# Performance work log

Hardware: AMD Instinct MI355X
Metric: run time of the kernel (lower is better)

The kernel has to match this reference:

```python
import jax, jax.numpy as jnp
import numpy as np

V, E, D, H = 50000, 800000, 128, 128  # nodes, edges, node_feat_size, graph_feat_size
NEG_SLOPE = 0.01  # nn.LeakyReLU default


def setup_inputs() -> dict:
    key = jax.random.key(0)
    ks = jax.random.split(key, 11)
    s = 0.05
    return {
        "node_feats": jax.random.normal(ks[0], (V, D), jnp.float32),
        "W_edge": jax.random.normal(ks[1], (1, 2 * D), jnp.float32) * s,
        "b_edge": jnp.zeros((1,), jnp.float32),
        "W_proj": jax.random.normal(ks[2], (H, D), jnp.float32) * s,
        "b_proj": jnp.zeros((H,), jnp.float32),
        "W_ih": jax.random.normal(ks[3], (3 * D, H), jnp.float32) * s,
        "W_hh": jax.random.normal(ks[4], (3 * D, D), jnp.float32) * s,
        "b_ih": jnp.zeros((3 * D,), jnp.float32),
        "b_hh": jnp.zeros((3 * D,), jnp.float32),
        "src": jax.random.randint(ks[5], (E,), 0, V),
        "dst": jax.random.randint(ks[6], (E,), 0, V),
    }


def _leaky_relu(x):
    return jnp.where(x >= 0, x, NEG_SLOPE * x)


def _edge_softmax(logits, dst, num_nodes):
    # segment softmax over edges grouped by destination node; logits: [E, 1]
    m = jax.ops.segment_max(logits, dst, num_segments=num_nodes)
    m = jnp.where(jnp.isfinite(m), m, 0.0)  # guard empty segments
    e = jnp.exp(logits - m[dst])
    s = jax.ops.segment_sum(e, dst, num_segments=num_nodes)
    return e / s[dst]


def reference(node_feats, W_edge, b_edge, W_proj, b_proj, W_ih, W_hh, b_ih, b_hh, src, dst):
    # GNNLayer.apply_edges: he = cat([dst_feat, src_feat])  [E, 2D]
    he = jnp.concatenate([node_feats[dst], node_feats[src]], axis=1)
    # project_edge: Dropout (eval: identity) -> Linear(2D, 1) -> LeakyReLU
    logits = _leaky_relu(he @ W_edge.T + b_edge)  # [E, 1]
    # AttentiveGRU2: edge_softmax per dst
    a = _edge_softmax(logits, dst, V)  # [E, 1]
    # project_node: Dropout (eval) -> Linear(D, H)
    hv = node_feats @ W_proj.T + b_proj  # [V, H]
    # src_mul_edge + sum aggregation to dst
    m = hv[src] * a  # [E, H]
    c = jax.ops.segment_sum(m, dst, num_segments=V)  # [V, H]
    context = jax.nn.elu(c)
    # PyTorch GRUCell(context, node_feats)
    gi = context @ W_ih.T + b_ih      # [V, 3D]
    gh = node_feats @ W_hh.T + b_hh   # [V, 3D]
    i_r, i_z, i_n = jnp.split(gi, 3, axis=1)
    h_r, h_z, h_n = jnp.split(gh, 3, axis=1)
    r = jax.nn.sigmoid(i_r + h_r)
    z = jax.nn.sigmoid(i_z + h_z)
    n = jnp.tanh(i_n + r * h_n)
    h_new = (1.0 - z) * n + z * node_feats
    return jax.nn.relu(h_new)
```

## Files before the change

kernel.cpp:

```cpp
#include <hip/hip_runtime.h>
#include <hip/hip_bf16.h>


#define V_NODES 50000
#define E_EDGES 800000
#define D_FEAT  128
#define GCHUNK  5
#define WS_BLOCKS 1250
#define GRU_BLOCKS 1264

#define NCHUNK  49
#define CHUNK_E 16384
#define RANGES  4
#define NODE_R  12500
#define HISTG   (NCHUNK * RANGES)
#define SCAN_BLOCKS 196

typedef short bf16x8 __attribute__((ext_vector_type(8)));
typedef float f32x4  __attribute__((ext_vector_type(4)));
typedef unsigned short u16x4 __attribute__((ext_vector_type(4)));

#define OFF_WEDGE 0
#define OFF_WPROJ 256
#define OFF_WIH   16640
#define OFF_WHH   65792
#define OFF_BEDGE 114944
#define OFF_BPROJ 114945
#define OFF_BIH   115073
#define OFF_BHH   115457
#define SMALL_TOTAL 115841
#define CONV_X_BLOCKS   6250
#define CONV_S_BLOCKS   453
#define HIST_BLOCKS     3125

__device__ int   g_is_bf16;
__device__ float g_pd[V_NODES];
__device__ float g_ps[V_NODES];
__device__ __attribute__((aligned(16))) unsigned int g_mat[NCHUNK * V_NODES];
__device__ int   g_row_off[V_NODES + 1];
__device__ int   g_blocksum[SCAN_BLOCKS];
__device__ unsigned short g_rank16[E_EDGES];
__device__ __attribute__((aligned(16))) int2 g_s_pair[E_EDGES];
__device__ __attribute__((aligned(16))) unsigned short g_xbf[V_NODES * D_FEAT];
__device__ __attribute__((aligned(16))) unsigned short g_wsmall[SMALL_TOTAL + 15];
__device__ __attribute__((aligned(16))) unsigned short g_hv[V_NODES * D_FEAT];
__device__ __attribute__((aligned(16))) unsigned short g_ctx[V_NODES * D_FEAT];

static __device__ __forceinline__ float b2f(unsigned short u) {
  union { unsigned int i; float f; } v; v.i = ((unsigned int)u) << 16; return v.f;
}
static __device__ __forceinline__ unsigned short f2b(float f) {
  unsigned int i = __float_as_uint(f);
  unsigned int r = (i + 0x7FFFu + ((i >> 16) & 1u)) >> 16;
  return (unsigned short)r;
}
static __device__ __forceinline__ bf16x8 load_frag(const unsigned short* p) {
  return *reinterpret_cast<const bf16x8*>(p);
}
static __device__ __forceinline__ float fast_rcp(float x) {
  return __builtin_amdgcn_rcpf(x);
}
static __device__ __forceinline__ float fast_sigmoid(float x) {
  return fast_rcp(1.f + __expf(-x));
}
static __device__ __forceinline__ float fast_tanh(float y) {
  return 1.f - 2.f * fast_rcp(__expf(2.f * y) + 1.f);
}
static __device__ __forceinline__ void async_copy16(const void* g, void* l) {
  __builtin_amdgcn_global_load_lds(
      (const __attribute__((address_space(1))) void*)g,
      (__attribute__((address_space(3))) void*)l, 16, 0, 0);
}

__global__ void probe_kernel(const unsigned int* __restrict__ x)
{
  __shared__ int cnt;
  if (threadIdx.x == 0) cnt = 0;
  __syncthreads();
  const unsigned int w  = x[threadIdx.x];
  const unsigned int lo = w & 0xFFFFu;
  const unsigned int ex = (lo >> 7) & 0xFFu;
  if (lo != 0u && ex >= 118u && ex <= 132u) atomicAdd(&cnt, 1);
  __syncthreads();
  if (threadIdx.x == 0) g_is_bf16 = (cnt >= 200) ? 1 : 0;
}

__global__ void conv_fused_kernel(
    const void* __restrict__ x,
    const void* p0, const void* p1, const void* p2, const void* p3,
    const void* p4, const void* p5, const void* p6, const void* p7)
{
  const int b = blockIdx.x;
  if (b < CONV_X_BLOCKS) {
    const int t = b * 256 + threadIdx.x;
    if (g_is_bf16) {
      reinterpret_cast<u16x4*>(g_xbf)[t] = reinterpret_cast<const u16x4*>(x)[t];
    } else {
      const float4 v = reinterpret_cast<const float4*>(x)[t];
      u16x4 o; o.x = f2b(v.x); o.y = f2b(v.y); o.z = f2b(v.z); o.w = f2b(v.w);
      reinterpret_cast<u16x4*>(g_xbf)[t] = o;
    }
  } else {
    const int i = (b - CONV_X_BLOCKS) * 256 + threadIdx.x;
    if (i >= SMALL_TOTAL) return;
    const int offs[9] = {OFF_WEDGE, OFF_WPROJ, OFF_WIH, OFF_WHH,
                         OFF_BEDGE, OFF_BPROJ, OFF_BIH, OFF_BHH, SMALL_TOTAL};
    const void* ps[8] = {p0, p1, p2, p3, p4, p5, p6, p7};
    int r = 0;
#pragma unroll
    for (int k = 0; k < 8; k++) if (i >= offs[k]) r = k;
    const int j = i - offs[r];
    g_wsmall[i] = g_is_bf16
        ? reinterpret_cast<const unsigned short*>(ps[r])[j]
        : f2b(reinterpret_cast<const float*>(ps[r])[j]);
  }
}

__global__ __launch_bounds__(256, 2) void np_hist_kernel(const int* __restrict__ dst)
{
  __shared__ unsigned int hloc[NODE_R / 2];
  __shared__ __attribute__((aligned(16))) char lds_x[2][4096];
  const int b = blockIdx.x;
  if (b < HISTG) {
    const int c  = b >> 2;
    const int r0 = (b & 3) * NODE_R;
    for (int i = threadIdx.x; i < NODE_R / 2; i += 256) hloc[i] = 0u;
    __syncthreads();
    const int ebase = c * CHUNK_E;
    const int ecnt  = min(CHUNK_E, E_EDGES - ebase);
    const int4* dst4 = reinterpret_cast<const int4*>(dst + ebase);
    const int n4 = ecnt >> 2;
    for (int i = threadIdx.x; i < n4; i += 256) {
      const int4 d4 = dst4[i];
      const int e0 = ebase + (i << 2);
      const unsigned int rx = (unsigned int)(d4.x - r0);
      const unsigned int ry = (unsigned int)(d4.y - r0);
      const unsigned int rz = (unsigned int)(d4.z - r0);
      const unsigned int rw = (unsigned int)(d4.w - r0);
      if (rx < (unsigned int)NODE_R) {
        const unsigned int sh = (rx & 1u) << 4;
        const unsigned int old = atomicAdd(&hloc[rx >> 1], 1u << sh);
        g_rank16[e0] = (unsigned short)((old >> sh) & 0xFFFFu);
      }
      if (ry < (unsigned int)NODE_R) {
        const unsigned int sh = (ry & 1u) << 4;
        const unsigned int old = atomicAdd(&hloc[ry >> 1], 1u << sh);
        g_rank16[e0 + 1] = (unsigned short)((old >> sh) & 0xFFFFu);
      }
      if (rz < (unsigned int)NODE_R) {
        const unsigned int sh = (rz & 1u) << 4;
        const unsigned int old = atomicAdd(&hloc[rz >> 1], 1u << sh);
        g_rank16[e0 + 2] = (unsigned short)((old >> sh) & 0xFFFFu);
      }
      if (rw < (unsigned int)NODE_R) {
        const unsigned int sh = (rw & 1u) << 4;
        const unsigned int old = atomicAdd(&hloc[rw >> 1], 1u << sh);
        g_rank16[e0 + 3] = (unsigned short)((old >> sh) & 0xFFFFu);
      }
    }
    __syncthreads();
    uint2* mout = reinterpret_cast<uint2*>(&g_mat[c * V_NODES + r0]);
    for (int i = threadIdx.x; i < NODE_R / 2; i += 256) {
      const unsigned int w = hloc[i];
      mout[i] = make_uint2(w & 0xFFFFu, w >> 16);
    }
    return;
  }
  const int wid   = threadIdx.x >> 6;
  const int g     = (b - HISTG) * 4 + wid;
  const int lane  = threadIdx.x & 63;
  const int cg    = g & 7;
  const int chunk = g >> 3;
  const int col   = lane & 15;
  const int quad  = lane >> 4;
  const int h     = 16 * cg + col;

  bf16x8 bw[4];
#pragma unroll
  for (int kk = 0; kk < 4; kk++)
    bw[kk] = load_frag(g_wsmall + OFF_WPROJ + h * D_FEAT + kk * 32 + quad * 8);
  bf16x8 be[4];
#pragma unroll
  for (int kk = 0; kk < 4; kk++) { be[kk] = bf16x8{0,0,0,0,0,0,0,0}; }
  if (cg == 0 && col < 2) {
#pragma unroll
    for (int kk = 0; kk < 4; kk++)
      be[kk] = load_frag(g_wsmall + OFF_WEDGE + col * D_FEAT + kk * 32 + quad * 8);
  }
  const float bp = b2f(g_wsmall[OFF_BPROJ + h]);

  const int o_lin = wid * 1024 + lane * 16;
  const int o_src = o_lin ^ (((o_lin >> 8) & 7) << 4);
  const char* xbf_b = reinterpret_cast<const char*>(g_xbf);

  const int t0 = chunk * GCHUNK;
  async_copy16(xbf_b + (size_t)t0 * 4096 + o_src, &lds_x[0][wid * 1024]);

  for (int i = 0; i < GCHUNK; i++) {
    const int t = t0 + i;
    const int buf = i & 1;
    __syncthreads();
    bf16x8 a[4];
#pragma unroll
    for (int kk = 0; kk < 4; kk++) {
      const int phys = (col * 256 + kk * 64 + quad * 16) ^ ((col & 7) << 4);
      a[kk] = *reinterpret_cast<const bf16x8*>(&lds_x[buf][phys]);
    }
    if (i + 1 < GCHUNK)
      async_copy16(xbf_b + (size_t)(t + 1) * 4096 + o_src,
                   &lds_x[buf ^ 1][wid * 1024]);
    f32x4 acc; acc[0]=0.f; acc[1]=0.f; acc[2]=0.f; acc[3]=0.f;
#pragma unroll
    for (int kk = 0; kk < 4; kk++)
      acc = __builtin_amdgcn_mfma_f32_16x16x32_bf16(a[kk], bw[kk], acc, 0, 0, 0);
#pragma unroll
    for (int r = 0; r < 4; r++)
      g_hv[(t * 16 + quad * 4 + r) * D_FEAT + h] = f2b(acc[r] + bp);
    if (cg == 0) {
      f32x4 acce; acce[0]=0.f; acce[1]=0.f; acce[2]=0.f; acce[3]=0.f;
#pragma unroll
      for (int kk = 0; kk < 4; kk++)
        acce = __builtin_amdgcn_mfma_f32_16x16x32_bf16(a[kk], be[kk], acce, 0, 0, 0);
      if (col == 0) {
#pragma unroll
        for (int r = 0; r < 4; r++) g_pd[t * 16 + quad * 4 + r] = acce[r];
      } else if (col == 1) {
#pragma unroll
        for (int r = 0; r < 4; r++) g_ps[t * 16 + quad * 4 + r] = acce[r];
      }
    }
  }
}

__global__ __launch_bounds__(256) void scan_a_kernel()
{
  __shared__ int lds[256];
  const int b = blockIdx.x, t = threadIdx.x;
  const int idx = b * 256 + t;
  int v = 0;
  if (idx < V_NODES) {
#pragma unroll 7
    for (int c = 0; c < NCHUNK; c++) v += (int)g_mat[c * V_NODES + idx];
  }
  lds[t] = v;
  __syncthreads();
  for (int off = 1; off < 256; off <<= 1) {
    int tmp = (t >= off) ? lds[t - off] : 0;
    __syncthreads();
    lds[t] += tmp;
    __syncthreads();
  }
  if (idx < V_NODES) g_row_off[idx] = lds[t] - v;
  if (t == 255) g_blocksum[b] = lds[255];
}

__global__ __launch_bounds__(256) void scan_bcm_kernel()
{
  __shared__ int lds[256];
  const int b = blockIdx.x, t = threadIdx.x;
  const int v = (t < SCAN_BLOCKS) ? g_blocksum[t] : 0;
  lds[t] = v;
  __syncthreads();
  for (int off = 1; off < 256; off <<= 1) {
    int tmp = (t >= off) ? lds[t - off] : 0;
    __syncthreads();
    lds[t] += tmp;
    __syncthreads();
  }
  const int total = lds[255];
  const int boff  = (b == 0) ? 0 : lds[b - 1];
  const int idx = b * 256 + t;
  if (idx < V_NODES) {
    int running = g_row_off[idx] + boff;
    g_row_off[idx] = running;
#pragma unroll 7
    for (int c = 0; c < NCHUNK; c++) {
      const unsigned int cnt = g_mat[c * V_NODES + idx];
      g_mat[c * V_NODES + idx] = (unsigned int)running;
      running += (int)cnt;
    }
  }
  if (b == 0 && t == 0) g_row_off[V_NODES] = total;
}

__global__ void edge_scatter_kernel(
    const int* __restrict__ src, const int* __restrict__ dst, int E)
{
  int e = blockIdx.x * blockDim.x + threadIdx.x;
  if (e >= E) return;
  const int d = dst[e], sn = src[e];
  float logit = g_pd[d] + g_ps[sn] + b2f(g_wsmall[OFF_BEDGE]);
  logit = (logit >= 0.f) ? logit : 0.01f * logit;
  const float w = __expf(logit);
  const int c = e >> 14;
  const int pos = (int)g_mat[c * V_NODES + d] + (int)g_rank16[e];
  g_s_pair[pos] = make_int2(sn, __float_as_int(w));
}

__global__ __launch_bounds__(256) void aggregate_kernel()
{
  const int v = blockIdx.x * 4 + (threadIdx.x >> 6);
  const int lane = threadIdx.x & 63;
  const int beg = g_row_off[v], end = g_row_off[v + 1];
  float accx = 0.f, accy = 0.f, ssum = 0.f;
  int i = beg;
  for (; i + 8 <= end; i += 8) {
    int2 q[8];
#pragma unroll
    for (int j = 0; j < 8; j++) q[j] = g_s_pair[i + j];
    unsigned int p[8];
#pragma unroll
    for (int j = 0; j < 8; j++)
      p[j] = *reinterpret_cast<const unsigned int*>(g_hv + q[j].x * D_FEAT + lane * 2);
#pragma unroll
    for (int j = 0; j < 8; j++) {
      const float w = __int_as_float(q[j].y);
      ssum += w;
      accx += w * b2f((unsigned short)(p[j] & 0xFFFFu));
      accy += w * b2f((unsigned short)(p[j] >> 16));
    }
  }
  for (; i + 4 <= end; i += 4) {
    int2 q[4];
#pragma unroll
    for (int j = 0; j < 4; j++) q[j] = g_s_pair[i + j];
    unsigned int p[4];
#pragma unroll
    for (int j = 0; j < 4; j++)
      p[j] = *reinterpret_cast<const unsigned int*>(g_hv + q[j].x * D_FEAT + lane * 2);
#pragma unroll
    for (int j = 0; j < 4; j++) {
      const float w = __int_as_float(q[j].y);
      ssum += w;
      accx += w * b2f((unsigned short)(p[j] & 0xFFFFu));
      accy += w * b2f((unsigned short)(p[j] >> 16));
    }
  }
  for (; i < end; i++) {
    const int2 q = g_s_pair[i];
    const float w = __int_as_float(q.y);
    ssum += w;
    const unsigned int pair =
        *reinterpret_cast<const unsigned int*>(g_hv + q.x * D_FEAT + lane * 2);
    accx += w * b2f((unsigned short)(pair & 0xFFFFu));
    accy += w * b2f((unsigned short)(pair >> 16));
  }
  const float inv = (end > beg) ? (1.0f / ssum) : 0.0f;
  float c0 = accx * inv, c1 = accy * inv;
  c0 = (c0 > 0.f) ? c0 : (__expf(c0) - 1.f);
  c1 = (c1 > 0.f) ? c1 : (__expf(c1) - 1.f);
  const unsigned int outp = ((unsigned int)f2b(c1) << 16) | (unsigned int)f2b(c0);
  *reinterpret_cast<unsigned int*>(g_ctx + v * D_FEAT + lane * 2) = outp;
}

__global__ __launch_bounds__(256, 2) void gru_kernel(const float* __restrict__ xf32,
                                                     float* __restrict__ out)
{
  const int d = blockIdx.x;
  const int x = d & 7;
  const int s = d >> 3;
  const int chunk = x + 8 * (s >> 1);
  if (chunk >= 625) return;
  __shared__ __attribute__((aligned(16))) char lds_s[2][8192];
  const int half  = s & 1;
  const int wid   = threadIdx.x >> 6;
  const int lane  = threadIdx.x & 63;
  const int cg    = half * 4 + wid;
  const int col   = lane & 15;
  const int quad  = lane >> 4;
  const int h     = 16 * cg + col;
  const unsigned short* W_ih = g_wsmall + OFF_WIH;
  const unsigned short* W_hh = g_wsmall + OFF_WHH;
  const int isb = g_is_bf16;

  const float br  = b2f(g_wsmall[OFF_BIH + h])       + b2f(g_wsmall[OFF_BHH + h]);
  const float bz  = b2f(g_wsmall[OFF_BIH + 128 + h]) + b2f(g_wsmall[OFF_BHH + 128 + h]);
  const float bn  = b2f(g_wsmall[OFF_BIH + 256 + h]);
  const float bh_ = b2f(g_wsmall[OFF_BHH + 256 + h]);

  bf16x8 bIHr[4], bHHr[4], bIHz[4], bHHz[4], bIHn[4], bHHn[4];
#pragma unroll
  for (int kk = 0; kk < 4; kk++) {
    const int ko = kk * 32 + quad * 8;
    bIHr[kk] = load_frag(W_ih + h * D_FEAT + ko);
    bHHr[kk] = load_frag(W_hh + h * D_FEAT + ko);
    bIHz[kk] = load_frag(W_ih + (128 + h) * D_FEAT + ko);
    bHHz[kk] = load_frag(W_hh + (128 + h) * D_FEAT + ko);
    bIHn[kk] = load_frag(W_ih + (256 + h) * D_FEAT + ko);
    bHHn[kk] = load_frag(W_hh + (256 + h) * D_FEAT + ko);
  }

  const int o_lin = wid * 1024 + lane * 16;
  const int o_src = o_lin ^ (((o_lin >> 8) & 7) << 4);
  const char* xbf_b = reinterpret_cast<const char*>(g_xbf);
  const char* ctx_b = reinterpret_cast<const char*>(g_ctx);

  const int t0 = chunk * GCHUNK;
  async_copy16(xbf_b + (size_t)t0 * 4096 + o_src, &lds_s[0][wid * 1024]);
  async_copy16(ctx_b + (size_t)t0 * 4096 + o_src, &lds_s[0][4096 + wid * 1024]);

  for (int i = 0; i < GCHUNK; i++) {
    const int t = t0 + i;
    const int buf = i & 1;
    __syncthreads();
    bf16x8 ax[4], ac[4];
#pragma unroll
    for (int kk = 0; kk < 4; kk++) {
      const int phys = (col * 256 + kk * 64 + quad * 16) ^ ((col & 7) << 4);
      ax[kk] = *reinterpret_cast<const bf16x8*>(&lds_s[buf][phys]);
      ac[kk] = *reinterpret_cast<const bf16x8*>(&lds_s[buf][4096 + phys]);
    }
    if (i + 1 < GCHUNK) {
      async_copy16(xbf_b + (size_t)(t + 1) * 4096 + o_src,
                   &lds_s[buf ^ 1][wid * 1024]);
      async_copy16(ctx_b + (size_t)(t + 1) * 4096 + o_src,
                   &lds_s[buf ^ 1][4096 + wid * 1024]);
    }
    float xv[4];
    if (isb) {
#pragma unroll
      for (int r = 0; r < 4; r++)
        xv[r] = b2f(g_xbf[(t * 16 + quad * 4 + r) * D_FEAT + h]);
    } else {
#pragma unroll
      for (int r = 0; r < 4; r++)
        xv[r] = xf32[(t * 16 + quad * 4 + r) * D_FEAT + h];
    }
    f32x4 racc, zacc, niacc, nhacc;
    racc[0]=br;  racc[1]=br;  racc[2]=br;  racc[3]=br;
    zacc[0]=bz;  zacc[1]=bz;  zacc[2]=bz;  zacc[3]=bz;
    niacc[0]=bn; niacc[1]=bn; niacc[2]=bn; niacc[3]=bn;
    nhacc[0]=bh_; nhacc[1]=bh_; nhacc[2]=bh_; nhacc[3]=bh_;
#pragma unroll
    for (int kk = 0; kk < 4; kk++) {
      racc  = __builtin_amdgcn_mfma_f32_16x16x32_bf16(ac[kk], bIHr[kk], racc, 0, 0, 0);
      racc  = __builtin_amdgcn_mfma_f32_16x16x32_bf16(ax[kk], bHHr[kk], racc, 0, 0, 0);
      zacc  = __builtin_amdgcn_mfma_f32_16x16x32_bf16(ac[kk], bIHz[kk], zacc, 0, 0, 0);
      zacc  = __builtin_amdgcn_mfma_f32_16x16x32_bf16(ax[kk], bHHz[kk], zacc, 0, 0, 0);
      niacc = __builtin_amdgcn_mfma_f32_16x16x32_bf16(ac[kk], bIHn[kk], niacc, 0, 0, 0);
      nhacc = __builtin_amdgcn_mfma_f32_16x16x32_bf16(ax[kk], bHHn[kk], nhacc, 0, 0, 0);
    }
#pragma unroll
    for (int r = 0; r < 4; r++) {
      const int vrow = t * 16 + quad * 4 + r;
      const float rg = fast_sigmoid(racc[r]);
      const float zg = fast_sigmoid(zacc[r]);
      const float n  = fast_tanh(niacc[r] + rg * nhacc[r]);
      const float hn = (1.f - zg) * n + zg * xv[r];
      out[vrow * D_FEAT + h] = (hn < 0.f) ? 0.f : hn;
    }
  }
}

extern "C" void kernel_launch(void* const* d_in, const int* in_sizes, int n_in,
                              void* d_out, int out_size, void* d_ws, size_t ws_size,
                              hipStream_t stream)
{
  (void)d_ws; (void)ws_size; (void)out_size;

  int ix = -1, iWe = -1, ibe = -1, iWp = -1, ibp = -1,
      iWih = -1, iWhh = -1, ibih = -1, ibhh = -1, isrc = -1, idst = -1;
  for (int i = 0; i < n_in; i++) {
    const int s = in_sizes[i];
    if      (s == 6400000) ix = i;
    else if (s == 256)     iWe = i;
    else if (s == 1)       ibe = i;
    else if (s == 16384)   iWp = i;
    else if (s == 128)     ibp = i;
    else if (s == 49152)   { if (iWih < 0) iWih = i; else iWhh = i; }
    else if (s == 384)     { if (ibih < 0) ibih = i; else ibhh = i; }
    else if (s == 800000)  { if (isrc < 0) isrc = i; else idst = i; }
  }
  if (ix < 0 || iWe < 0 || ibe < 0 || iWp < 0 || ibp < 0 || iWih < 0 ||
      iWhh < 0 || ibih < 0 || ibhh < 0 || isrc < 0 || idst < 0) {
    ix = 0; iWe = 1; ibe = 2; iWp = 3; ibp = 4;
    iWih = 5; iWhh = 6; ibih = 7; ibhh = 8; isrc = 9; idst = 10;
  }

  const int* src = (const int*)d_in[isrc];
  const int* dst = (const int*)d_in[idst];
  float* out = (float*)d_out;

  probe_kernel<<<1, 256, 0, stream>>>((const unsigned int*)d_in[ix]);
  conv_fused_kernel<<<CONV_X_BLOCKS + CONV_S_BLOCKS, 256, 0, stream>>>(
      d_in[ix],
      d_in[iWe], d_in[iWp], d_in[iWih], d_in[iWhh],
      d_in[ibe], d_in[ibp], d_in[ibih], d_in[ibhh]);
  np_hist_kernel<<<HISTG + WS_BLOCKS, 256, 0, stream>>>(dst);
  scan_a_kernel<<<SCAN_BLOCKS, 256, 0, stream>>>();
  scan_bcm_kernel<<<SCAN_BLOCKS, 256, 0, stream>>>();
  edge_scatter_kernel<<<HIST_BLOCKS, 256, 0, stream>>>(src, dst, E_EDGES);
  aggregate_kernel<<<V_NODES / 4, 256, 0, stream>>>();
  gru_kernel<<<GRU_BLOCKS, 256, 0, stream>>>((const float*)d_in[ix], out);
}
```

Baseline: 207.2 us.

## Inline dtype probe per block, fuse conversion with histogram, deepen aggregate unroll

Removes the single-block probe kernel by having every conversion block and every GRU block recompute the bf16/fp32 detection locally from the first 256 input words. The dst histogram moves out of the node-projection kernel into the conversion kernel, so histogramming runs alongside format conversion and one launch plus one global flag disappear. The aggregate loop's gather batch grows from 8 to 12 edges to keep more loads in flight. In exchange every block pays an extra barrier pair and a small read, and the larger unroll raises register pressure.

```diff
diff --git a/kernel.cpp b/kernel.cpp
--- a/kernel.cpp
+++ b/kernel.cpp
@@ -33,7 +33,6 @@
 #define CONV_S_BLOCKS   453
 #define HIST_BLOCKS     3125
 
-__device__ int   g_is_bf16;
 __device__ float g_pd[V_NODES];
 __device__ float g_ps[V_NODES];
 __device__ __attribute__((aligned(16))) unsigned int g_mat[NCHUNK * V_NODES];
@@ -71,103 +70,104 @@
       (const __attribute__((address_space(1))) void*)g,
       (__attribute__((address_space(3))) void*)l, 16, 0, 0);
 }
-
-__global__ void probe_kernel(const unsigned int* __restrict__ x)
-{
-  __shared__ int cnt;
-  if (threadIdx.x == 0) cnt = 0;
-  __syncthreads();
-  const unsigned int w  = x[threadIdx.x];
+static __device__ __forceinline__ int block_probe(const unsigned int* xw,
+                                                  int* pcnt) {
+  if (threadIdx.x == 0) *pcnt = 0;
+  __syncthreads();
+  const unsigned int w  = xw[threadIdx.x];
   const unsigned int lo = w & 0xFFFFu;
   const unsigned int ex = (lo >> 7) & 0xFFu;
-  if (lo != 0u && ex >= 118u && ex <= 132u) atomicAdd(&cnt, 1);
-  __syncthreads();
-  if (threadIdx.x == 0) g_is_bf16 = (cnt >= 200) ? 1 : 0;
-}
-
-__global__ void conv_fused_kernel(
-    const void* __restrict__ x,
+  if (lo != 0u && ex >= 118u && ex <= 132u) atomicAdd(pcnt, 1);
+  __syncthreads();
+  return (*pcnt >= 200) ? 1 : 0;
+}
+
+__global__ __launch_bounds__(256, 2) void conv_hist_kernel(
+    const void* __restrict__ x, const int* __restrict__ dst,
     const void* p0, const void* p1, const void* p2, const void* p3,
     const void* p4, const void* p5, const void* p6, const void* p7)
 {
+  __shared__ unsigned int hloc[NODE_R / 2];
   const int b = blockIdx.x;
-  if (b < CONV_X_BLOCKS) {
-    const int t = b * 256 + threadIdx.x;
-    if (g_is_bf16) {
-      reinterpret_cast<u16x4*>(g_xbf)[t] = reinterpret_cast<const u16x4*>(x)[t];
+  if (b < CONV_X_BLOCKS + CONV_S_BLOCKS) {
+    const int isb = block_probe(reinterpret_cast<const unsigned int*>(x),
+                                reinterpret_cast<int*>(&hloc[0]));
+    if (b < CONV_X_BLOCKS) {
+      const int t = b * 256 + threadIdx.x;
+      if (isb) {
+        reinterpret_cast<u16x4*>(g_xbf)[t] = reinterpret_cast<const u16x4*>(x)[t];
+      } else {
+        const float4 v = reinterpret_cast<const float4*>(x)[t];
+        u16x4 o; o.x = f2b(v.x); o.y = f2b(v.y); o.z = f2b(v.z); o.w = f2b(v.w);
+        reinterpret_cast<u16x4*>(g_xbf)[t] = o;
+      }
     } else {
-      const float4 v = reinterpret_cast<const float4*>(x)[t];
-      u16x4 o; o.x = f2b(v.x); o.y = f2b(v.y); o.z = f2b(v.z); o.w = f2b(v.w);
-      reinterpret_cast<u16x4*>(g_xbf)[t] = o;
-    }
-  } else {
-    const int i = (b - CONV_X_BLOCKS) * 256 + threadIdx.x;
-    if (i >= SMALL_TOTAL) return;
-    const int offs[9] = {OFF_WEDGE, OFF_WPROJ, OFF_WIH, OFF_WHH,
-                         OFF_BEDGE, OFF_BPROJ, OFF_BIH, OFF_BHH, SMALL_TOTAL};
-    const void* ps[8] = {p0, p1, p2, p3, p4, p5, p6, p7};
-    int r = 0;
-#pragma unroll
-    for (int k = 0; k < 8; k++) if (i >= offs[k]) r = k;
-    const int j = i - offs[r];
-    g_wsmall[i] = g_is_bf16
-        ? reinterpret_cast<const unsigned short*>(ps[r])[j]
-        : f2b(reinterpret_cast<const float*>(ps[r])[j]);
-  }
-}
-
-__global__ __launch_bounds__(256, 2) void np_hist_kernel(const int* __restrict__ dst)
-{
-  __shared__ unsigned int hloc[NODE_R / 2];
+      const int i = (b - CONV_X_BLOCKS) * 256 + threadIdx.x;
+      if (i >= SMALL_TOTAL) return;
+      const int offs[9] = {OFF_WEDGE, OFF_WPROJ, OFF_WIH, OFF_WHH,
+                           OFF_BEDGE, OFF_BPROJ, OFF_BIH, OFF_BHH, SMALL_TOTAL};
+      const void* ps[8] = {p0, p1, p2, p3, p4, p5, p6, p7};
+      int r = 0;
+#pragma unroll
+      for (int k = 0; k < 8; k++) if (i >= offs[k]) r = k;
+      const int j = i - offs[r];
+      g_wsmall[i] = isb
+          ? reinterpret_cast<const unsigned short*>(ps[r])[j]
+          : f2b(reinterpret_cast<const float*>(ps[r])[j]);
+    }
+    return;
+  }
+  const int hb = b - CONV_X_BLOCKS - CONV_S_BLOCKS;
+  const int c  = hb >> 2;
+  const int r0 = (hb & 3) * NODE_R;
+  for (int i = threadIdx.x; i < NODE_R / 2; i += 256) hloc[i] = 0u;
+  __syncthreads();
+  const int ebase = c * CHUNK_E;
+  const int ecnt  = min(CHUNK_E, E_EDGES - ebase);
+  const int4* dst4 = reinterpret_cast<const int4*>(dst + ebase);
+  const int n4 = ecnt >> 2;
+  for (int i = threadIdx.x; i < n4; i += 256) {
+    const int4 d4 = dst4[i];
+    const int e0 = ebase + (i << 2);
+    const unsigned int rx = (unsigned int)(d4.x - r0);
+    const unsigned int ry = (unsigned int)(d4.y - r0);
+    const unsigned int rz = (unsigned int)(d4.z - r0);
+    const unsigned int rw = (unsigned int)(d4.w - r0);
+    if (rx < (unsigned int)NODE_R) {
+      const unsigned int sh = (rx & 1u) << 4;
+      const unsigned int old = atomicAdd(&hloc[rx >> 1], 1u << sh);
+      g_rank16[e0] = (unsigned short)((old >> sh) & 0xFFFFu);
+    }
+    if (ry < (unsigned int)NODE_R) {
+      const unsigned int sh = (ry & 1u) << 4;
+      const unsigned int old = atomicAdd(&hloc[ry >> 1], 1u << sh);
+      g_rank16[e0 + 1] = (unsigned short)((old >> sh) & 0xFFFFu);
+    }
+    if (rz < (unsigned int)NODE_R) {
+      const unsigned int sh = (rz & 1u) << 4;
+      const unsigned int old = atomicAdd(&hloc[rz >> 1], 1u << sh);
+      g_rank16[e0 + 2] = (unsigned short)((old >> sh) & 0xFFFFu);
+    }
+    if (rw < (unsigned int)NODE_R) {
+      const unsigned int sh = (rw & 1u) << 4;
+      const unsigned int old = atomicAdd(&hloc[rw >> 1], 1u << sh);
+      g_rank16[e0 + 3] = (unsigned short)((old >> sh) & 0xFFFFu);
+    }
+  }
+  __syncthreads();
+  uint2* mout = reinterpret_cast<uint2*>(&g_mat[c * V_NODES + r0]);
+  for (int i = threadIdx.x; i < NODE_R / 2; i += 256) {
+    const unsigned int w = hloc[i];
+    mout[i] = make_uint2(w & 0xFFFFu, w >> 16);
+  }
+}
+
+__global__ __launch_bounds__(256, 2) void np_kernel()
+{
   __shared__ __attribute__((aligned(16))) char lds_x[2][4096];
   const int b = blockIdx.x;
-  if (b < HISTG) {
-    const int c  = b >> 2;
-    const int r0 = (b & 3) * NODE_R;
-    for (int i = threadIdx.x; i < NODE_R / 2; i += 256) hloc[i] = 0u;
-    __syncthreads();
-    const int ebase = c * CHUNK_E;
-    const int ecnt  = min(CHUNK_E, E_EDGES - ebase);
-    const int4* dst4 = reinterpret_cast<const int4*>(dst + ebase);
-    const int n4 = ecnt >> 2;
-    for (int i = threadIdx.x; i < n4; i += 256) {
-      const int4 d4 = dst4[i];
-      const int e0 = ebase + (i << 2);
-      const unsigned int rx = (unsigned int)(d4.x - r0);
-      const unsigned int ry = (unsigned int)(d4.y - r0);
-      const unsigned int rz = (unsigned int)(d4.z - r0);
-      const unsigned int rw = (unsigned int)(d4.w - r0);
-      if (rx < (unsigned int)NODE_R) {
-        const unsigned int sh = (rx & 1u) << 4;
-        const unsigned int old = atomicAdd(&hloc[rx >> 1], 1u << sh);
-        g_rank16[e0] = (unsigned short)((old >> sh) & 0xFFFFu);
-      }
-      if (ry < (unsigned int)NODE_R) {
-        const unsigned int sh = (ry & 1u) << 4;
-        const unsigned int old = atomicAdd(&hloc[ry >> 1], 1u << sh);
-        g_rank16[e0 + 1] = (unsigned short)((old >> sh) & 0xFFFFu);
-      }
-      if (rz < (unsigned int)NODE_R) {
-        const unsigned int sh = (rz & 1u) << 4;
-        const unsigned int old = atomicAdd(&hloc[rz >> 1], 1u << sh);
-        g_rank16[e0 + 2] = (unsigned short)((old >> sh) & 0xFFFFu);
-      }
-      if (rw < (unsigned int)NODE_R) {
-        const unsigned int sh = (rw & 1u) << 4;
-        const unsigned int old = atomicAdd(&hloc[rw >> 1], 1u << sh);
-        g_rank16[e0 + 3] = (unsigned short)((old >> sh) & 0xFFFFu);
-      }
-    }
-    __syncthreads();
-    uint2* mout = reinterpret_cast<uint2*>(&g_mat[c * V_NODES + r0]);
-    for (int i = threadIdx.x; i < NODE_R / 2; i += 256) {
-      const unsigned int w = hloc[i];
-      mout[i] = make_uint2(w & 0xFFFFu, w >> 16);
-    }
-    return;
-  }
   const int wid   = threadIdx.x >> 6;
-  const int g     = (b - HISTG) * 4 + wid;
+  const int g     = b * 4 + wid;
   const int lane  = threadIdx.x & 63;
   const int cg    = g & 7;
   const int chunk = g >> 3;
@@ -304,16 +304,16 @@
   const int beg = g_row_off[v], end = g_row_off[v + 1];
   float accx = 0.f, accy = 0.f, ssum = 0.f;
   int i = beg;
-  for (; i + 8 <= end; i += 8) {
-    int2 q[8];
-#pragma unroll
-    for (int j = 0; j < 8; j++) q[j] = g_s_pair[i + j];
-    unsigned int p[8];
-#pragma unroll
-    for (int j = 0; j < 8; j++)
+  for (; i + 12 <= end; i += 12) {
+    int2 q[12];
+#pragma unroll
+    for (int j = 0; j < 12; j++) q[j] = g_s_pair[i + j];
+    unsigned int p[12];
+#pragma unroll
+    for (int j = 0; j < 12; j++)
       p[j] = *reinterpret_cast<const unsigned int*>(g_hv + q[j].x * D_FEAT + lane * 2);
 #pragma unroll
-    for (int j = 0; j < 8; j++) {
+    for (int j = 0; j < 12; j++) {
       const float w = __int_as_float(q[j].y);
       ssum += w;
       accx += w * b2f((unsigned short)(p[j] & 0xFFFFu));
@@ -362,6 +362,8 @@
   const int chunk = x + 8 * (s >> 1);
   if (chunk >= 625) return;
   __shared__ __attribute__((aligned(16))) char lds_s[2][8192];
+  __shared__ int pcnt;
+  const int isb = block_probe(reinterpret_cast<const unsigned int*>(xf32), &pcnt);
   const int half  = s & 1;
   const int wid   = threadIdx.x >> 6;
   const int lane  = threadIdx.x & 63;
@@ -371,7 +373,6 @@
   const int h     = 16 * cg + col;
   const unsigned short* W_ih = g_wsmall + OFF_WIH;
   const unsigned short* W_hh = g_wsmall + OFF_WHH;
-  const int isb = g_is_bf16;
 
   const float br  = b2f(g_wsmall[OFF_BIH + h])       + b2f(g_wsmall[OFF_BHH + h]);
   const float bz  = b2f(g_wsmall[OFF_BIH + 128 + h]) + b2f(g_wsmall[OFF_BHH + 128 + h]);
@@ -481,12 +482,11 @@
   const int* dst = (const int*)d_in[idst];
   float* out = (float*)d_out;
 
-  probe_kernel<<<1, 256, 0, stream>>>((const unsigned int*)d_in[ix]);
-  conv_fused_kernel<<<CONV_X_BLOCKS + CONV_S_BLOCKS, 256, 0, stream>>>(
-      d_in[ix],
+  conv_hist_kernel<<<CONV_X_BLOCKS + CONV_S_BLOCKS + HISTG, 256, 0, stream>>>(
+      d_in[ix], dst,
       d_in[iWe], d_in[iWp], d_in[iWih], d_in[iWhh],
       d_in[ibe], d_in[ibp], d_in[ibih], d_in[ibhh]);
-  np_hist_kernel<<<HISTG + WS_BLOCKS, 256, 0, stream>>>(dst);
+  np_kernel<<<WS_BLOCKS, 256, 0, stream>>>();
   scan_a_kernel<<<SCAN_BLOCKS, 256, 0, stream>>>();
   scan_bcm_kernel<<<SCAN_BLOCKS, 256, 0, stream>>>();
   edge_scatter_kernel<<<HIST_BLOCKS, 256, 0, stream>>>(src, dst, E_EDGES);
```

Measured after the change: 219.1 us. 1.06x slower.
